# Optimization experiments

Hardware: AMD Instinct MI355X
Metric: run time of the kernel (lower is better)

The kernel has to match this reference:

```python
import math
import jax, jax.numpy as jnp
import numpy as np
from jax import lax

FS = 16000.0
TAU_FAST_MS = 2.0
TAU_SLOW_MS = 60.0
EPS = 1e-6


def setup_inputs() -> dict:
    key = jax.random.key(0)
    B, C, T = 8, 64, 64000
    x = jax.random.normal(key, (B, C, T), dtype=jnp.float32)
    mu_fast = jnp.float32(1.0 - math.exp(-1.0 / (FS * TAU_FAST_MS / 1000.0)))
    mu_slow = jnp.float32(1.0 - math.exp(-1.0 / (FS * TAU_SLOW_MS / 1000.0)))
    mix_weight_adapt = jnp.float32(0.5)
    mix_weight_hp = jnp.float32(0.3)
    return {
        "x": x,
        "mu_fast": mu_fast,
        "mu_slow": mu_slow,
        "mix_weight_adapt": mix_weight_adapt,
        "mix_weight_hp": mix_weight_hp,
    }


def reference(x, mu_fast, mu_slow, mix_weight_adapt, mix_weight_hp):
    # x: [B, C, T]
    x = jnp.maximum(x, 0.0)
    xt = jnp.moveaxis(x, -1, 0)  # [T, B, C], time-leading for scan

    def step(carry, xcur):
        mf, ms = carry
        mf = (1.0 - mu_fast) * mf + mu_fast * xcur
        ms = (1.0 - mu_slow) * ms + mu_slow * xcur
        return (mf, ms), (mf, ms)

    init = (xt[0], xt[0])  # EMA initialized at first sample
    _, (mf_rest, ms_rest) = lax.scan(step, init, xt[1:])
    M_fast = jnp.concatenate([xt[:1], mf_rest], axis=0)  # [T, B, C]
    M_slow = jnp.concatenate([xt[:1], ms_rest], axis=0)

    mix_adapt = jax.nn.sigmoid(mix_weight_adapt)
    M = mix_adapt * M_fast + (1.0 - mix_adapt) * M_slow
    M = jnp.moveaxis(M, 0, -1)  # back to [B, C, T]

    x_adapted = x / (EPS + M)
    x_hp = x - M
    mix_hp = jax.nn.sigmoid(mix_weight_hp)
    return x_adapted + mix_hp * x_hp
```

## Files before the change

### kernel.cpp

```cpp
#include <hip/hip_runtime.h>


#define THREADS 256
#define WPB 4
#define K 25
#define WTILE (64 * K)
#define T_LEN 64000
#define SEGS_W 4
#define SEG_LEN (T_LEN / SEGS_W)
#define SEG_TILES (SEG_LEN / WTILE)
#define HALO_TILES 4
#define EPS_V 1e-6f

__global__ __launch_bounds__(THREADS, 3)
void dual_ema_hp_kernel(const float* __restrict__ x,
                        const float* __restrict__ p_mu_fast,
                        const float* __restrict__ p_mu_slow,
                        const float* __restrict__ p_mwa,
                        const float* __restrict__ p_mhp,
                        float* __restrict__ out)
{
    __shared__ float lds[WPB * 2 * WTILE];
    const int tid  = threadIdx.x;
    const int lane = tid & 63;
    const int wv   = tid >> 6;
    float* ibuf = &lds[wv * 2 * WTILE];
    float* obuf = ibuf + WTILE;

    const int gw  = blockIdx.x * WPB + wv;
    const int row = gw / SEGS_W;
    const int seg = gw % SEGS_W;
    const int h   = (seg == 0) ? 0 : HALO_TILES;
    const int nt  = SEG_TILES + h;

    const float* gseg = x   + (size_t)row * T_LEN + (size_t)seg * SEG_LEN - (size_t)h * WTILE;
    float*       oseg = out + (size_t)row * T_LEN + (size_t)seg * SEG_LEN - (size_t)h * WTILE;

    const float mu_f = p_mu_fast[0];
    const float mu_s = p_mu_slow[0];
    const float af = 1.0f - mu_f;
    const float as = 1.0f - mu_s;
    const float wa  = 1.0f / (1.0f + __expf(-p_mwa[0]));
    const float wb  = 1.0f - wa;
    const float whp = 1.0f / (1.0f + __expf(-p_mhp[0]));

    const float Pf1  = __powf(af, (float)K);
    const float Ps1  = __powf(as, (float)K);
    const float Pf2  = Pf1 * Pf1,   Ps2  = Ps1 * Ps1;
    const float Pf4  = Pf2 * Pf2,   Ps4  = Ps2 * Ps2;
    const float Pf8  = Pf4 * Pf4,   Ps8  = Ps4 * Ps4;
    const float Pf16 = Pf8 * Pf8,   Ps16 = Ps8 * Ps8;
    const float Pf32 = Pf16 * Pf16, Ps32 = Ps16 * Ps16;

    float4 p0, p1, p2, p3, p4, p5; float ps;
    {
        const float4* g4 = (const float4*)gseg;
        p0 = g4[0 * 64 + lane]; p1 = g4[1 * 64 + lane]; p2 = g4[2 * 64 + lane];
        p3 = g4[3 * 64 + lane]; p4 = g4[4 * 64 + lane]; p5 = g4[5 * 64 + lane];
        ps = gseg[1536 + lane];
    }
    {
        float4* i4 = (float4*)ibuf;
        i4[0 * 64 + lane] = p0; i4[1 * 64 + lane] = p1; i4[2 * 64 + lane] = p2;
        i4[3 * 64 + lane] = p3; i4[4 * 64 + lane] = p4; i4[5 * 64 + lane] = p5;
        ibuf[1536 + lane] = ps;
    }

    float sfr = 0.0f, ssr = 0.0f;

    for (int t = 0; t < nt; ++t) {
        asm volatile("s_waitcnt lgkmcnt(0)" ::: "memory");
        float y[K];
#pragma unroll
        for (int i = 0; i < K; ++i)
            y[i] = fmaxf(ibuf[lane * K + i], 0.0f);

        const bool pref = (t + 1 < nt);
        if (pref) {
            const float* gt = gseg + (size_t)(t + 1) * WTILE;
            const float4* g4 = (const float4*)gt;
            p0 = g4[0 * 64 + lane]; p1 = g4[1 * 64 + lane]; p2 = g4[2 * 64 + lane];
            p3 = g4[3 * 64 + lane]; p4 = g4[4 * 64 + lane]; p5 = g4[5 * 64 + lane];
            ps = gt[1536 + lane];
        }

        if (seg == 0 && t == 0 && lane == 0) { sfr = y[0]; ssr = y[0]; }

        float inf = (lane == 0) ? sfr : 0.0f;
        float ins = (lane == 0) ? ssr : 0.0f;
        float mf = fmaf(af, inf, mu_f * y[0]);
        float ms = fmaf(as, ins, mu_s * y[0]);
#pragma unroll
        for (int i = 1; i < K; ++i) {
            mf = fmaf(af, mf, mu_f * y[i]);
            ms = fmaf(as, ms, mu_s * y[i]);
        }

        float cf = mf, cs = ms, uf, us;
        uf = __shfl_up(cf, 1);  us = __shfl_up(cs, 1);
        cf = (lane >= 1)  ? fmaf(Pf1,  uf, cf) : cf;  cs = (lane >= 1)  ? fmaf(Ps1,  us, cs) : cs;
        uf = __shfl_up(cf, 2);  us = __shfl_up(cs, 2);
        cf = (lane >= 2)  ? fmaf(Pf2,  uf, cf) : cf;  cs = (lane >= 2)  ? fmaf(Ps2,  us, cs) : cs;
        uf = __shfl_up(cf, 4);  us = __shfl_up(cs, 4);
        cf = (lane >= 4)  ? fmaf(Pf4,  uf, cf) : cf;  cs = (lane >= 4)  ? fmaf(Ps4,  us, cs) : cs;
        uf = __shfl_up(cf, 8);  us = __shfl_up(cs, 8);
        cf = (lane >= 8)  ? fmaf(Pf8,  uf, cf) : cf;  cs = (lane >= 8)  ? fmaf(Ps8,  us, cs) : cs;
        uf = __shfl_up(cf, 16); us = __shfl_up(cs, 16);
        cf = (lane >= 16) ? fmaf(Pf16, uf, cf) : cf;  cs = (lane >= 16) ? fmaf(Ps16, us, cs) : cs;
        uf = __shfl_up(cf, 32); us = __shfl_up(cs, 32);
        cf = (lane >= 32) ? fmaf(Pf32, uf, cf) : cf;  cs = (lane >= 32) ? fmaf(Ps32, us, cs) : cs;

        float ex_f = __shfl_up(cf, 1), ex_s = __shfl_up(cs, 1);
        if (lane == 0) { ex_f = sfr; ex_s = ssr; }
        sfr = __shfl(cf, 63);
        ssr = __shfl(cs, 63);

        if (t >= h) {
            float mf2 = ex_f, ms2 = ex_s;
#pragma unroll
            for (int i = 0; i < K; ++i) {
                float yv = y[i];
                mf2 = fmaf(af, mf2, mu_f * yv);
                ms2 = fmaf(as, ms2, mu_s * yv);
                float M = fmaf(wa, mf2, wb * ms2);
                float o = yv * __builtin_amdgcn_rcpf(EPS_V + M) + whp * (yv - M);
                obuf[lane * K + i] = o;
            }
            asm volatile("s_waitcnt lgkmcnt(0)" ::: "memory");

            float* gout = oseg + (size_t)t * WTILE;
            float4* go4 = (float4*)gout;
            const float4* o4 = (const float4*)obuf;
            go4[0 * 64 + lane] = o4[0 * 64 + lane];
            go4[1 * 64 + lane] = o4[1 * 64 + lane];
            go4[2 * 64 + lane] = o4[2 * 64 + lane];
            go4[3 * 64 + lane] = o4[3 * 64 + lane];
            go4[4 * 64 + lane] = o4[4 * 64 + lane];
            go4[5 * 64 + lane] = o4[5 * 64 + lane];
            gout[1536 + lane] = obuf[1536 + lane];
        }

        if (pref) {
            float4* i4 = (float4*)ibuf;
            i4[0 * 64 + lane] = p0; i4[1 * 64 + lane] = p1; i4[2 * 64 + lane] = p2;
            i4[3 * 64 + lane] = p3; i4[4 * 64 + lane] = p4; i4[5 * 64 + lane] = p5;
            ibuf[1536 + lane] = ps;
        }
    }
}

extern "C" void kernel_launch(void* const* d_in, const int* in_sizes, int n_in,
                              void* d_out, int out_size, void* d_ws, size_t ws_size,
                              hipStream_t stream) {
    const float* x    = (const float*)d_in[0];
    const float* mu_f = (const float*)d_in[1];
    const float* mu_s = (const float*)d_in[2];
    const float* mwa  = (const float*)d_in[3];
    const float* mhp  = (const float*)d_in[4];
    float* out = (float*)d_out;

    const int rows   = in_sizes[0] / T_LEN;
    const int blocks = rows * SEGS_W / WPB;
    dual_ema_hp_kernel<<<blocks, THREADS, 0, stream>>>(x, mu_f, mu_s, mwa, mhp, out);
}
```

Baseline: 247.8 us.

## Share one LDS buffer for input and output tiles, double segments per row

Merges each wave's separate input and output LDS buffers into one, halving shared memory per block, and raises the occupancy hint from 3 to 4 blocks. The computed output is read back from LDS into registers before the next prefetched input overwrites the buffer, and the global stores are issued after that. Segments per row go from 4 to 8, which doubles the number of waves but also doubles the halo recomputation overhead. Holding the output in registers adds register pressure, which may conflict with the higher occupancy target.

```diff
diff --git a/kernel.cpp b/kernel.cpp
--- a/kernel.cpp
+++ b/kernel.cpp
@@ -6,13 +6,13 @@
 #define K 25
 #define WTILE (64 * K)
 #define T_LEN 64000
-#define SEGS_W 4
+#define SEGS_W 8
 #define SEG_LEN (T_LEN / SEGS_W)
 #define SEG_TILES (SEG_LEN / WTILE)
 #define HALO_TILES 4
 #define EPS_V 1e-6f
 
-__global__ __launch_bounds__(THREADS, 3)
+__global__ __launch_bounds__(THREADS, 4)
 void dual_ema_hp_kernel(const float* __restrict__ x,
                         const float* __restrict__ p_mu_fast,
                         const float* __restrict__ p_mu_slow,
@@ -20,12 +20,11 @@
                         const float* __restrict__ p_mhp,
                         float* __restrict__ out)
 {
-    __shared__ float lds[WPB * 2 * WTILE];
+    __shared__ float lds[WPB * WTILE];
     const int tid  = threadIdx.x;
     const int lane = tid & 63;
     const int wv   = tid >> 6;
-    float* ibuf = &lds[wv * 2 * WTILE];
-    float* obuf = ibuf + WTILE;
+    float* buf = &lds[wv * WTILE];
 
     const int gw  = blockIdx.x * WPB + wv;
     const int row = gw / SEGS_W;
@@ -60,10 +59,10 @@
         ps = gseg[1536 + lane];
     }
     {
-        float4* i4 = (float4*)ibuf;
+        float4* i4 = (float4*)buf;
         i4[0 * 64 + lane] = p0; i4[1 * 64 + lane] = p1; i4[2 * 64 + lane] = p2;
         i4[3 * 64 + lane] = p3; i4[4 * 64 + lane] = p4; i4[5 * 64 + lane] = p5;
-        ibuf[1536 + lane] = ps;
+        buf[1536 + lane] = ps;
     }
 
     float sfr = 0.0f, ssr = 0.0f;
@@ -73,7 +72,7 @@
         float y[K];
 #pragma unroll
         for (int i = 0; i < K; ++i)
-            y[i] = fmaxf(ibuf[lane * K + i], 0.0f);
+            y[i] = fmaxf(buf[lane * K + i], 0.0f);
 
         const bool pref = (t + 1 < nt);
         if (pref) {
@@ -115,7 +114,9 @@
         sfr = __shfl(cf, 63);
         ssr = __shfl(cs, 63);
 
-        if (t >= h) {
+        const bool emit = (t >= h);
+        float4 s0, s1, s2, s3, s4, s5; float ss;
+        if (emit) {
             float mf2 = ex_f, ms2 = ex_s;
 #pragma unroll
             for (int i = 0; i < K; ++i) {
@@ -124,27 +125,33 @@
                 ms2 = fmaf(as, ms2, mu_s * yv);
                 float M = fmaf(wa, mf2, wb * ms2);
                 float o = yv * __builtin_amdgcn_rcpf(EPS_V + M) + whp * (yv - M);
-                obuf[lane * K + i] = o;
+                buf[lane * K + i] = o;
             }
             asm volatile("s_waitcnt lgkmcnt(0)" ::: "memory");
 
-            float* gout = oseg + (size_t)t * WTILE;
-            float4* go4 = (float4*)gout;
-            const float4* o4 = (const float4*)obuf;
-            go4[0 * 64 + lane] = o4[0 * 64 + lane];
-            go4[1 * 64 + lane] = o4[1 * 64 + lane];
-            go4[2 * 64 + lane] = o4[2 * 64 + lane];
-            go4[3 * 64 + lane] = o4[3 * 64 + lane];
-            go4[4 * 64 + lane] = o4[4 * 64 + lane];
-            go4[5 * 64 + lane] = o4[5 * 64 + lane];
-            gout[1536 + lane] = obuf[1536 + lane];
+            const float4* o4 = (const float4*)buf;
+            s0 = o4[0 * 64 + lane]; s1 = o4[1 * 64 + lane]; s2 = o4[2 * 64 + lane];
+            s3 = o4[3 * 64 + lane]; s4 = o4[4 * 64 + lane]; s5 = o4[5 * 64 + lane];
+            ss = buf[1536 + lane];
         }
 
         if (pref) {
-            float4* i4 = (float4*)ibuf;
+            float4* i4 = (float4*)buf;
             i4[0 * 64 + lane] = p0; i4[1 * 64 + lane] = p1; i4[2 * 64 + lane] = p2;
             i4[3 * 64 + lane] = p3; i4[4 * 64 + lane] = p4; i4[5 * 64 + lane] = p5;
-            ibuf[1536 + lane] = ps;
+            buf[1536 + lane] = ps;
+        }
+
+        if (emit) {
+            float* gout = oseg + (size_t)t * WTILE;
+            float4* go4 = (float4*)gout;
+            go4[0 * 64 + lane] = s0;
+            go4[1 * 64 + lane] = s1;
+            go4[2 * 64 + lane] = s2;
+            go4[3 * 64 + lane] = s3;
+            go4[4 * 64 + lane] = s4;
+            go4[5 * 64 + lane] = s5;
+            gout[1536 + lane] = ss;
         }
     }
 }
```

After: 324.2 us. 30.8% more time.
